# Kernel optimization log

Measured on AMD Instinct MI355X. Metric: run time of the kernel, lower is better.

## Reference

```python
import jax, jax.numpy as jnp
import numpy as np

VW, VD, VH = 96, 96, 96  # voxel_width, voxel_depth, voxel_height


def _grid_points():
    # voxel centers mapped to [-1, 1]: (2*i + 1 - N) / N
    xp = (2.0 * jnp.arange(VW) + 1.0 - VW) / VW
    yp = (2.0 * jnp.arange(VD) + 1.0 - VD) / VD
    zp = (2.0 * jnp.arange(VH) + 1.0 - VH) / VH
    X, Y, Z = jnp.meshgrid(xp, yp, zp, indexing='ij')
    return jnp.stack([X.ravel(), Y.ravel(), Z.ravel()], axis=-1)  # (V, 3)


def setup_inputs() -> dict:
    key = jax.random.key(0)
    k1, k2 = jax.random.split(key)
    B, NV, NF = 8, 2048, 512
    vertices = jax.random.uniform(k1, (B, NV, 3), dtype=jnp.float32, minval=-1.0, maxval=1.0)
    facets = jax.random.randint(k2, (B, NF, 4), 0, NV, dtype=jnp.int64)
    return {"vertices": vertices, "facets": facets}


def reference(vertices, facets):
    # vertices: (B, NV, 3) float32; facets: (B, NF, 4) int indices into vertices
    B = vertices.shape[0]
    NF = facets.shape[1]
    # vertices_to_facets: per-batch gather -> (B, NF, 4, 3)
    fverts = jax.vmap(lambda v, f: v[f])(vertices, facets)
    P = _grid_points()                      # (V, 3) voxel centers
    V = P.shape[0]

    def step(idx_map, xs):
        fi, verts = xs                      # verts: (B, 4, 3)
        v3 = verts[:, 3]                    # (B, 3)
        # T[:, j] = verts[j] - verts[3]  (columns are tetra edges)
        T = jnp.swapaxes(verts[:, :3] - v3[:, None, :], 1, 2)  # (B, 3, 3)
        a, b, c = T[:, 0, 0], T[:, 0, 1], T[:, 0, 2]
        d, e, f = T[:, 1, 0], T[:, 1, 1], T[:, 1, 2]
        g, h, i = T[:, 2, 0], T[:, 2, 1], T[:, 2, 2]
        # adjugate of T (matches t_inv_* in the original)
        adj = jnp.stack([
            jnp.stack([e * i - f * h, c * h - b * i, b * f - c * e], axis=-1),
            jnp.stack([f * g - d * i, a * i - c * g, c * d - a * f], axis=-1),
            jnp.stack([d * h - e * g, b * g - a * h, a * e - b * d], axis=-1),
        ], axis=1)                          # (B, 3, 3)
        det = a * (e * i - f * h) - b * (d * i - f * g) + c * (d * h - e * g)  # (B,)
        dvec = P[None, :, :] - v3[:, None, :]                  # (B, V, 3)
        lam = jnp.einsum('brc,bvc->bvr', adj, dvec) / det[:, None, None]  # (B, V, 3)
        lam4 = 1.0 - lam.sum(axis=-1, keepdims=True)
        lams = jnp.concatenate([lam, lam4], axis=-1)           # (B, V, 4)
        # original skips when any lambda < 0 or > 1 (strict) -> inside is inclusive
        inside = jnp.all((lams >= 0.0) & (lams <= 1.0), axis=-1)  # (B, V)
        idx_map = jnp.where((idx_map < 0) & inside, fi, idx_map)
        return idx_map, None

    idx0 = jnp.full((B, V), -1, dtype=jnp.int32)
    xs = (jnp.arange(NF, dtype=jnp.int32), jnp.swapaxes(fverts, 0, 1))
    idx_map, _ = jax.lax.scan(step, idx0, xs)
    alpha = (idx_map >= 0).astype(jnp.float32).reshape(B, VW, VD, VH)
    return alpha
```

## Files before the change

kernel.cpp:

```cpp
#include <hip/hip_runtime.h>

#pragma clang fp contract(off)

#define VWD 96
#define NVERT 2048
#define NFAC 512
#define NBATCH 8
#define NSLAB 3456
#define RECF 16
#define CULC 22

#define CUL(c, b, f) cul[(size_t)(c) * (NBATCH * NFAC) + (size_t)(b) * NFAC + (f)]

__global__ __launch_bounds__(512) void precompute_kernel(
    const float* __restrict__ vertices,
    const int*   __restrict__ facets,
    float*       __restrict__ cul,
    float*       __restrict__ body)
{
    __shared__ unsigned skey[NFAC];
    const int b = blockIdx.x;
    const int j = threadIdx.x;
    const float* vb = vertices + (size_t)b * NVERT * 3;

    int4 fi = ((const int4*)facets)[b * NFAC + j];
    float x0 = vb[3*fi.x+0], y0 = vb[3*fi.x+1], z0 = vb[3*fi.x+2];
    float x1 = vb[3*fi.y+0], y1 = vb[3*fi.y+1], z1 = vb[3*fi.y+2];
    float x2 = vb[3*fi.z+0], y2 = vb[3*fi.z+1], z2 = vb[3*fi.z+2];
    float x3 = vb[3*fi.w+0], y3 = vb[3*fi.w+1], z3 = vb[3*fi.w+2];
    float a  = x0-x3, bb = x1-x3, c  = x2-x3;
    float d  = y0-y3, e  = y1-y3, f  = y2-y3;
    float g  = z0-z3, h  = z1-z3, ii = z2-z3;
    float A00 = e*ii - f*h,  A01 = c*h  - bb*ii, A02 = bb*f - c*e;
    float A10 = f*g  - d*ii, A11 = a*ii - c*g,   A12 = c*d  - a*f;
    float A20 = d*h  - e*g,  A21 = bb*g - a*h,   A22 = a*e  - bb*d;
    float det = a*(e*ii - f*h) - bb*(d*ii - f*g) + c*(d*h - e*g);
    if (det < 0.0f) {
        det = -det;
        A00 = -A00; A01 = -A01; A02 = -A02;
        A10 = -A10; A11 = -A11; A12 = -A12;
        A20 = -A20; A21 = -A21; A22 = -A22;
    }
    unsigned myk = ~__float_as_uint(det);
    skey[j] = myk;
    __syncthreads();

    int rank = 0;
    const uint4* sk4 = (const uint4*)skey;
    for (int k0 = 0; k0 < NFAC; k0 += 4) {
        uint4 kk = sk4[k0 >> 2];
        rank += (kk.x < myk) + ((kk.x == myk) & (k0 + 0 < j));
        rank += (kk.y < myk) + ((kk.y == myk) & (k0 + 1 < j));
        rank += (kk.z < myk) + ((kk.z == myk) & (k0 + 2 < j));
        rank += (kk.w < myk) + ((kk.w == myk) & (k0 + 3 < j));
    }

    CUL(0, b, rank) = fminf(fminf(x0,x1),fminf(x2,x3)) - 1e-4f;
    CUL(1, b, rank) = fminf(fminf(y0,y1),fminf(y2,y3)) - 1e-4f;
    CUL(2, b, rank) = fminf(fminf(z0,z1),fminf(z2,z3)) - 1e-4f;
    CUL(3, b, rank) = fmaxf(fmaxf(x0,x1),fmaxf(x2,x3)) + 1e-4f;
    CUL(4, b, rank) = fmaxf(fmaxf(y0,y1),fmaxf(y2,y3)) + 1e-4f;
    CUL(5, b, rank) = fmaxf(fmaxf(z0,z1),fmaxf(z2,z3)) + 1e-4f;

    const float HX = 7.0f/96.0f, HZ = 3.0f/96.0f;
    auto plane = [&](float pax, float pay, float paz,
                     float pbx, float pby, float pbz,
                     float pcx, float pcy, float pcz,
                     float pox, float poy, float poz, int base) {
        float e1x = pbx-pax, e1y = pby-pay, e1z = pbz-paz;
        float e2x = pcx-pax, e2y = pcy-pay, e2z = pcz-paz;
        float nx = e1y*e2z - e1z*e2y;
        float ny = e1z*e2x - e1x*e2z;
        float nz = e1x*e2y - e1y*e2x;
        float sdot = nx*(pox-pax) + ny*(poy-pay) + nz*(poz-paz);
        if (sdot > 0.0f) { nx=-nx; ny=-ny; nz=-nz; sdot=-sdot; }
        float dpl = nx*pax + ny*pay + nz*paz;
        float n1s = fabsf(nx)+fabsf(ny)+fabsf(nz);
        float M = 1e-4f*(-sdot) + 1e-4f*n1s + 1e-4f;
        float rhs = dpl + M + (fabsf(nx)*HX + fabsf(ny)*HX + fabsf(nz)*HZ);
        CUL(base+0, b, rank) = nx;
        CUL(base+1, b, rank) = ny;
        CUL(base+2, b, rank) = nz;
        CUL(base+3, b, rank) = rhs;
    };
    plane(x1,y1,z1, x2,y2,z2, x3,y3,z3, x0,y0,z0, 6);
    plane(x0,y0,z0, x2,y2,z2, x3,y3,z3, x1,y1,z1, 10);
    plane(x0,y0,z0, x1,y1,z1, x3,y3,z3, x2,y2,z2, 14);
    plane(x0,y0,z0, x1,y1,z1, x2,y2,z2, x3,y3,z3, 18);

    float* bo = body + ((size_t)b * NFAC + rank) * RECF;
    bo[0]  = det; bo[1]  = x3;  bo[2]  = y3;  bo[3]  = z3;
    bo[4]  = A00; bo[5]  = A01; bo[6]  = A02; bo[7]  = A10;
    bo[8]  = A11; bo[9]  = A12; bo[10] = A20; bo[11] = A21;
    bo[12] = A22;
    bo[13] = det * (1.0f - 1e-5f) - 1e-25f;
    bo[14] = det * (1.0f + 1e-5f) + 1e-25f;
    bo[15] = 0.0f;
}

__global__ __launch_bounds__(512) void mask_kernel(
    const float* __restrict__ cul,
    unsigned long long* __restrict__ masks)
{
    const int col = blockIdx.x;
    const int b   = blockIdx.y;
    const int f   = threadIdx.x;
    const int w   = threadIdx.x >> 6;
    float bminx=CUL(0,b,f), bminy=CUL(1,b,f), bminz=CUL(2,b,f);
    float bmaxx=CUL(3,b,f), bmaxy=CUL(4,b,f), bmaxz=CUL(5,b,f);
    float n0x=CUL(6,b,f),  n0y=CUL(7,b,f),  n0z=CUL(8,b,f),  r0=CUL(9,b,f);
    float n1x=CUL(10,b,f), n1y=CUL(11,b,f), n1z=CUL(12,b,f), r1=CUL(13,b,f);
    float n2x=CUL(14,b,f), n2y=CUL(15,b,f), n2z=CUL(16,b,f), r2=CUL(17,b,f);
    float n3x=CUL(18,b,f), n3y=CUL(19,b,f), n3z=CUL(20,b,f), r3=CUL(21,b,f);

    const int sx = col / 12, sy = col % 12;
    const float cx = (float)(16*sx + 8 - VWD) / 96.0f;
    const float cy = (float)(16*sy + 8 - VWD) / 96.0f;
    const float colminx = (float)(16*sx + 1  - VWD) / 96.0f;
    const float colmaxx = (float)(16*sx + 15 - VWD) / 96.0f;
    const float colminy = (float)(16*sy + 1  - VWD) / 96.0f;
    const float colmaxy = (float)(16*sy + 15 - VWD) / 96.0f;
    const bool ovxy = (bminx <= colmaxx) & (bmaxx >= colminx) &
                      (bminy <= colmaxy) & (bmaxy >= colminy);

    const float cz0   = (float)(4 - VWD) / 96.0f;
    const float stepc = 8.0f / 96.0f;
    float d0 = n0x*cx + n0y*cy + n0z*cz0 - r0;  float s0 = n0z*stepc;
    float d1 = n1x*cx + n1y*cy + n1z*cz0 - r1;  float s1 = n1z*stepc;
    float d2 = n2x*cx + n2y*cy + n2z*cz0 - r2;  float s2 = n2z*stepc;
    float d3 = n3x*cx + n3y*cy + n3z*cz0 - r3;  float s3 = n3z*stepc;
    float zlo = (float)(1 - VWD) / 96.0f;
    float zhi = (float)(7 - VWD) / 96.0f;

    unsigned long long* mp = masks + ((size_t)b * NSLAB + (size_t)col * 24) * 8 + w;
#pragma unroll 4
    for (int sz = 0; sz < 24; ++sz) {
        bool ov = ovxy & (bminz <= zhi) & (bmaxz >= zlo) &
                  (d0 <= 0.0f) & (d1 <= 0.0f) & (d2 <= 0.0f) & (d3 <= 0.0f);
        unsigned long long bal = __ballot((int)ov);
        if ((threadIdx.x & 63) == 0) mp[(size_t)sz * 8] = bal;
        d0 += s0; d1 += s1; d2 += s2; d3 += s3;
        zlo += stepc; zhi += stepc;
    }
}

__global__ __launch_bounds__(128) void voxelize_kernel(
    const float*              __restrict__ body,
    const unsigned long long* __restrict__ masks,
    float*                    __restrict__ out)
{
    const int b    = blockIdx.y;
    const int wave = threadIdx.x >> 6;
    const int lane = threadIdx.x & 63;
    const int slab = blockIdx.x * 2 + wave;
    const int sz = slab % 24;
    const int sy = (slab / 24) % 12;
    const int sx = slab / 288;
    const int ix  = sx*8 + (lane >> 3);
    const int iy  = sy*8 + (lane & 7);
    const int iz0 = sz*4;

    const float px  = (float)(2*ix + 1 - VWD) / 96.0f;
    const float py  = (float)(2*iy + 1 - VWD) / 96.0f;
    const float pz0 = (float)(2*(iz0+0) + 1 - VWD) / 96.0f;
    const float pz1 = (float)(2*(iz0+1) + 1 - VWD) / 96.0f;
    const float pz2 = (float)(2*(iz0+2) + 1 - VWD) / 96.0f;
    const float pz3 = (float)(2*(iz0+3) + 1 - VWD) / 96.0f;

    const unsigned long long* mp = masks + ((size_t)b * NSLAB + slab) * 8;
    const float* bb = body + (size_t)b * NFAC * RECF;

    unsigned fnd = 0u;
    for (int w = 0; w < 8; ++w) {
        unsigned long long m = mp[w];
        while (m) {
            int bit = __builtin_ctzll(m);
            m &= m - 1;
            int f = __builtin_amdgcn_readfirstlane(w * 64 + bit);
            const float* bo = bb + f * RECF;
            float det = bo[0], v3x = bo[1], v3y = bo[2], v3z = bo[3];
            float A00 = bo[4],  A01 = bo[5],  A02 = bo[6],  A10 = bo[7];
            float A11 = bo[8],  A12 = bo[9],  A20 = bo[10], A21 = bo[11];
            float A22 = bo[12], dhi = bo[13], mhi = bo[14];
            float dx = px - v3x, dy = py - v3y;
            float p0 = A00*dx + A01*dy;
            float p1 = A10*dx + A11*dy;
            float p2 = A20*dx + A21*dy;
            float dzk0 = pz0 - v3z, dzk1 = pz1 - v3z;
            float dzk2 = pz2 - v3z, dzk3 = pz3 - v3z;
            unsigned need = 0u;
#pragma unroll
            for (int k = 0; k < 4; ++k) {
                float dzk = (k == 0) ? dzk0 : (k == 1) ? dzk1
                          : (k == 2) ? dzk2 : dzk3;
                float n0 = p0 + A02*dzk;
                float n1 = p1 + A12*dzk;
                float n2 = p2 + A22*dzk;
                float sm = (n0 + n1) + n2;
                float mn = fminf(fminf(n0, n1), n2);
                bool ge0 = (mn >= 0.0f);
                bool def = ge0 & (sm <= dhi);
                bool may = ge0 & (sm <= mhi);
                if (may & !def & !((fnd >> k) & 1u)) need |= (1u << k);
                if (def) fnd |= (1u << k);
            }
            if (__any(need != 0u)) {
#pragma unroll
                for (int k = 0; k < 4; ++k) {
                    float dzk = (k == 0) ? dzk0 : (k == 1) ? dzk1
                              : (k == 2) ? dzk2 : dzk3;
                    float n0 = p0 + A02*dzk;
                    float n1 = p1 + A12*dzk;
                    float n2 = p2 + A22*dzk;
                    float l0 = n0 / det;
                    float l1 = n1 / det;
                    float l2 = n2 / det;
                    float l3 = 1.0f - ((l0 + l1) + l2);
                    bool inside = (l0 >= 0.0f) & (l0 <= 1.0f) &
                                  (l1 >= 0.0f) & (l1 <= 1.0f) &
                                  (l2 >= 0.0f) & (l2 <= 1.0f) &
                                  (l3 >= 0.0f) & (l3 <= 1.0f);
                    if (((need >> k) & 1u) & inside) fnd |= (1u << k);
                }
            }
            if (__all(fnd == 15u)) goto done;
        }
    }
done:
    float4 v;
    v.x = (fnd & 1u) ? 1.0f : 0.0f;
    v.y = (fnd & 2u) ? 1.0f : 0.0f;
    v.z = (fnd & 4u) ? 1.0f : 0.0f;
    v.w = (fnd & 8u) ? 1.0f : 0.0f;
    *(float4*)&out[(size_t)b*(VWD*VWD*VWD) + (size_t)ix*(VWD*VWD) + iy*VWD + iz0] = v;
}

extern "C" void kernel_launch(void* const* d_in, const int* in_sizes, int n_in,
                              void* d_out, int out_size, void* d_ws, size_t ws_size,
                              hipStream_t stream) {
    const float* vertices = (const float*)d_in[0];
    const int*   facets   = (const int*)d_in[1];
    float*       out      = (float*)d_out;

    float* cul  = (float*)d_ws;
    float* body = (float*)((char*)d_ws + (size_t)CULC * NBATCH * NFAC * 4);
    unsigned long long* msk =
        (unsigned long long*)((char*)d_ws +
                              (size_t)(CULC + RECF) * NBATCH * NFAC * 4);

    precompute_kernel<<<NBATCH, 512, 0, stream>>>(vertices, facets, cul, body);
    mask_kernel<<<dim3(144, NBATCH), 512, 0, stream>>>(cul, msk);
    dim3 grid(NSLAB / 2, NBATCH);
    voxelize_kernel<<<grid, 128, 0, stream>>>(body, msk, out);
}
```

Baseline: 144.8 us.

## Skip fully covered slabs and defer high-index facets to a compacted fix-up kernel

The mask kernel now records, per column and z-slab, whether some tetrahedron's planes provably contain the whole slab, using per-plane margin thresholds computed in precompute. Such slabs are written as all-ones without any per-facet tests. The main voxelize kernel only walks the first 128 facet bits. Slabs that still have unresolved voxels and remaining candidates are appended to a global list via atomics, and a new fix-up kernel processes them with six waves splitting the remaining facet words and sharing results through LDS atomics. This aims to cut long serial facet walks and improve load balance, at the cost of an extra launch, atomics, and a conservative coverage test that must stay exact.

```diff
diff --git a/kernel.cpp b/kernel.cpp
--- a/kernel.cpp
+++ b/kernel.cpp
@@ -8,7 +8,7 @@
 #define NBATCH 8
 #define NSLAB 3456
 #define RECF 16
-#define CULC 22
+#define CULC 26
 
 #define CUL(c, b, f) cul[(size_t)(c) * (NBATCH * NFAC) + (size_t)(b) * NFAC + (f)]
 
@@ -16,11 +16,13 @@
     const float* __restrict__ vertices,
     const int*   __restrict__ facets,
     float*       __restrict__ cul,
-    float*       __restrict__ body)
+    float*       __restrict__ body,
+    unsigned*    __restrict__ scnt)
 {
     __shared__ unsigned skey[NFAC];
     const int b = blockIdx.x;
     const int j = threadIdx.x;
+    if (b == 0 && j == 0) scnt[0] = 0u;
     const float* vb = vertices + (size_t)b * NVERT * 3;
 
     int4 fi = ((const int4*)facets)[b * NFAC + j];
@@ -66,7 +68,7 @@
     auto plane = [&](float pax, float pay, float paz,
                      float pbx, float pby, float pbz,
                      float pcx, float pcy, float pcz,
-                     float pox, float poy, float poz, int base) {
+                     float pox, float poy, float poz, int base, int pi) {
         float e1x = pbx-pax, e1y = pby-pay, e1z = pbz-paz;
         float e2x = pcx-pax, e2y = pcy-pay, e2z = pcz-paz;
         float nx = e1y*e2z - e1z*e2y;
@@ -77,16 +79,18 @@
         float dpl = nx*pax + ny*pay + nz*paz;
         float n1s = fabsf(nx)+fabsf(ny)+fabsf(nz);
         float M = 1e-4f*(-sdot) + 1e-4f*n1s + 1e-4f;
-        float rhs = dpl + M + (fabsf(nx)*HX + fabsf(ny)*HX + fabsf(nz)*HZ);
+        float E = fabsf(nx)*HX + fabsf(ny)*HX + fabsf(nz)*HZ;
+        float rhs = dpl + M + E;
         CUL(base+0, b, rank) = nx;
         CUL(base+1, b, rank) = ny;
         CUL(base+2, b, rank) = nz;
         CUL(base+3, b, rank) = rhs;
+        CUL(22+pi, b, rank) = -(M + 2.0f*E + 2e-3f);
     };
-    plane(x1,y1,z1, x2,y2,z2, x3,y3,z3, x0,y0,z0, 6);
-    plane(x0,y0,z0, x2,y2,z2, x3,y3,z3, x1,y1,z1, 10);
-    plane(x0,y0,z0, x1,y1,z1, x3,y3,z3, x2,y2,z2, 14);
-    plane(x0,y0,z0, x1,y1,z1, x2,y2,z2, x3,y3,z3, 18);
+    plane(x1,y1,z1, x2,y2,z2, x3,y3,z3, x0,y0,z0, 6, 0);
+    plane(x0,y0,z0, x2,y2,z2, x3,y3,z3, x1,y1,z1, 10, 1);
+    plane(x0,y0,z0, x1,y1,z1, x3,y3,z3, x2,y2,z2, 14, 2);
+    plane(x0,y0,z0, x1,y1,z1, x2,y2,z2, x3,y3,z3, 18, 3);
 
     float* bo = body + ((size_t)b * NFAC + rank) * RECF;
     bo[0]  = det; bo[1]  = x3;  bo[2]  = y3;  bo[3]  = z3;
@@ -100,18 +104,23 @@
 
 __global__ __launch_bounds__(512) void mask_kernel(
     const float* __restrict__ cul,
-    unsigned long long* __restrict__ masks)
-{
+    unsigned long long* __restrict__ masks,
+    unsigned* __restrict__ fullmask)
+{
+    __shared__ unsigned fullbits;
     const int col = blockIdx.x;
     const int b   = blockIdx.y;
     const int f   = threadIdx.x;
     const int w   = threadIdx.x >> 6;
+    if (threadIdx.x == 0) fullbits = 0u;
+    __syncthreads();
     float bminx=CUL(0,b,f), bminy=CUL(1,b,f), bminz=CUL(2,b,f);
     float bmaxx=CUL(3,b,f), bmaxy=CUL(4,b,f), bmaxz=CUL(5,b,f);
     float n0x=CUL(6,b,f),  n0y=CUL(7,b,f),  n0z=CUL(8,b,f),  r0=CUL(9,b,f);
     float n1x=CUL(10,b,f), n1y=CUL(11,b,f), n1z=CUL(12,b,f), r1=CUL(13,b,f);
     float n2x=CUL(14,b,f), n2y=CUL(15,b,f), n2z=CUL(16,b,f), r2=CUL(17,b,f);
     float n3x=CUL(18,b,f), n3y=CUL(19,b,f), n3z=CUL(20,b,f), r3=CUL(21,b,f);
+    float D0=CUL(22,b,f), D1=CUL(23,b,f), D2=CUL(24,b,f), D3=CUL(25,b,f);
 
     const int sx = col / 12, sy = col % 12;
     const float cx = (float)(16*sx + 8 - VWD) / 96.0f;
@@ -132,29 +141,91 @@
     float zlo = (float)(1 - VWD) / 96.0f;
     float zhi = (float)(7 - VWD) / 96.0f;
 
+    unsigned fullw = 0u;
     unsigned long long* mp = masks + ((size_t)b * NSLAB + (size_t)col * 24) * 8 + w;
 #pragma unroll 4
     for (int sz = 0; sz < 24; ++sz) {
         bool ov = ovxy & (bminz <= zhi) & (bmaxz >= zlo) &
                   (d0 <= 0.0f) & (d1 <= 0.0f) & (d2 <= 0.0f) & (d3 <= 0.0f);
+        bool fullv = (d0 <= D0) & (d1 <= D1) & (d2 <= D2) & (d3 <= D3);
         unsigned long long bal = __ballot((int)ov);
         if ((threadIdx.x & 63) == 0) mp[(size_t)sz * 8] = bal;
+        if (__ballot((int)fullv) != 0ull) fullw |= (1u << sz);
         d0 += s0; d1 += s1; d2 += s2; d3 += s3;
         zlo += stepc; zhi += stepc;
+    }
+    if ((threadIdx.x & 63) == 0 && fullw) atomicOr(&fullbits, fullw);
+    __syncthreads();
+    if (threadIdx.x == 0) fullmask[b * 144 + col] = fullbits;
+}
+
+__device__ __forceinline__ void facet_test(
+    const float* __restrict__ bo,
+    float px, float py, float pz0, float pz1, float pz2, float pz3,
+    unsigned& fnd)
+{
+    float det = bo[0], v3x = bo[1], v3y = bo[2], v3z = bo[3];
+    float A00 = bo[4],  A01 = bo[5],  A02 = bo[6],  A10 = bo[7];
+    float A11 = bo[8],  A12 = bo[9],  A20 = bo[10], A21 = bo[11];
+    float A22 = bo[12], dhi = bo[13], mhi = bo[14];
+    float dx = px - v3x, dy = py - v3y;
+    float p0 = A00*dx + A01*dy;
+    float p1 = A10*dx + A11*dy;
+    float p2 = A20*dx + A21*dy;
+    float dzk0 = pz0 - v3z, dzk1 = pz1 - v3z;
+    float dzk2 = pz2 - v3z, dzk3 = pz3 - v3z;
+    unsigned need = 0u;
+#pragma unroll
+    for (int k = 0; k < 4; ++k) {
+        float dzk = (k == 0) ? dzk0 : (k == 1) ? dzk1
+                  : (k == 2) ? dzk2 : dzk3;
+        float n0 = p0 + A02*dzk;
+        float n1 = p1 + A12*dzk;
+        float n2 = p2 + A22*dzk;
+        float sm = (n0 + n1) + n2;
+        float mn = fminf(fminf(n0, n1), n2);
+        bool ge0 = (mn >= 0.0f);
+        bool def = ge0 & (sm <= dhi);
+        bool may = ge0 & (sm <= mhi);
+        if (may & !def & !((fnd >> k) & 1u)) need |= (1u << k);
+        if (def) fnd |= (1u << k);
+    }
+    if (__any(need != 0u)) {
+#pragma unroll
+        for (int k = 0; k < 4; ++k) {
+            float dzk = (k == 0) ? dzk0 : (k == 1) ? dzk1
+                      : (k == 2) ? dzk2 : dzk3;
+            float n0 = p0 + A02*dzk;
+            float n1 = p1 + A12*dzk;
+            float n2 = p2 + A22*dzk;
+            float l0 = n0 / det;
+            float l1 = n1 / det;
+            float l2 = n2 / det;
+            float l3 = 1.0f - ((l0 + l1) + l2);
+            bool inside = (l0 >= 0.0f) & (l0 <= 1.0f) &
+                          (l1 >= 0.0f) & (l1 <= 1.0f) &
+                          (l2 >= 0.0f) & (l2 <= 1.0f) &
+                          (l3 >= 0.0f) & (l3 <= 1.0f);
+            if (((need >> k) & 1u) & inside) fnd |= (1u << k);
+        }
     }
 }
 
 __global__ __launch_bounds__(128) void voxelize_kernel(
     const float*              __restrict__ body,
     const unsigned long long* __restrict__ masks,
-    float*                    __restrict__ out)
+    const unsigned*           __restrict__ fullmask,
+    float*                    __restrict__ out,
+    unsigned*                 __restrict__ scnt,
+    unsigned short*           __restrict__ slist)
 {
     const int b    = blockIdx.y;
     const int wave = threadIdx.x >> 6;
     const int lane = threadIdx.x & 63;
     const int slab = blockIdx.x * 2 + wave;
     const int sz = slab % 24;
-    const int sy = (slab / 24) % 12;
+    const int col = slab / 24;
+    const int sy = col % 12;
     const int sx = slab / 288;
     const int ix  = sx*8 + (lane >> 3);
     const int iy  = sy*8 + (lane & 7);
@@ -167,63 +238,30 @@
     const float pz2 = (float)(2*(iz0+2) + 1 - VWD) / 96.0f;
     const float pz3 = (float)(2*(iz0+3) + 1 - VWD) / 96.0f;
 
-    const unsigned long long* mp = masks + ((size_t)b * NSLAB + slab) * 8;
-    const float* bb = body + (size_t)b * NFAC * RECF;
-
     unsigned fnd = 0u;
-    for (int w = 0; w < 8; ++w) {
-        unsigned long long m = mp[w];
-        while (m) {
-            int bit = __builtin_ctzll(m);
-            m &= m - 1;
-            int f = __builtin_amdgcn_readfirstlane(w * 64 + bit);
-            const float* bo = bb + f * RECF;
-            float det = bo[0], v3x = bo[1], v3y = bo[2], v3z = bo[3];
-            float A00 = bo[4],  A01 = bo[5],  A02 = bo[6],  A10 = bo[7];
-            float A11 = bo[8],  A12 = bo[9],  A20 = bo[10], A21 = bo[11];
-            float A22 = bo[12], dhi = bo[13], mhi = bo[14];
-            float dx = px - v3x, dy = py - v3y;
-            float p0 = A00*dx + A01*dy;
-            float p1 = A10*dx + A11*dy;
-            float p2 = A20*dx + A21*dy;
-            float dzk0 = pz0 - v3z, dzk1 = pz1 - v3z;
-            float dzk2 = pz2 - v3z, dzk3 = pz3 - v3z;
-            unsigned need = 0u;
+
+    if ((fullmask[b * 144 + col] >> sz) & 1u) { fnd = 15u; goto done; }
+
+    {
+        const unsigned long long* mp = masks + ((size_t)b * NSLAB + slab) * 8;
+        const float* bb = body + (size_t)b * NFAC * RECF;
 #pragma unroll
-            for (int k = 0; k < 4; ++k) {
-                float dzk = (k == 0) ? dzk0 : (k == 1) ? dzk1
-                          : (k == 2) ? dzk2 : dzk3;
-                float n0 = p0 + A02*dzk;
-                float n1 = p1 + A12*dzk;
-                float n2 = p2 + A22*dzk;
-                float sm = (n0 + n1) + n2;
-                float mn = fminf(fminf(n0, n1), n2);
-                bool ge0 = (mn >= 0.0f);
-                bool def = ge0 & (sm <= dhi);
-                bool may = ge0 & (sm <= mhi);
-                if (may & !def & !((fnd >> k) & 1u)) need |= (1u << k);
-                if (def) fnd |= (1u << k);
+        for (int w = 0; w < 2; ++w) {
+            unsigned long long m = mp[w];
+            while (m) {
+                int bit = __builtin_ctzll(m);
+                m &= m - 1;
+                int f = __builtin_amdgcn_readfirstlane(w * 64 + bit);
+                facet_test(bb + f * RECF, px, py, pz0, pz1, pz2, pz3, fnd);
+                if (__all(fnd == 15u)) goto done;
             }
-            if (__any(need != 0u)) {
-#pragma unroll
-                for (int k = 0; k < 4; ++k) {
-                    float dzk = (k == 0) ? dzk0 : (k == 1) ? dzk1
-                              : (k == 2) ? dzk2 : dzk3;
-                    float n0 = p0 + A02*dzk;
-                    float n1 = p1 + A12*dzk;
-                    float n2 = p2 + A22*dzk;
-                    float l0 = n0 / det;
-                    float l1 = n1 / det;
-                    float l2 = n2 / det;
-                    float l3 = 1.0f - ((l0 + l1) + l2);
-                    bool inside = (l0 >= 0.0f) & (l0 <= 1.0f) &
-                                  (l1 >= 0.0f) & (l1 <= 1.0f) &
-                                  (l2 >= 0.0f) & (l2 <= 1.0f) &
-                                  (l3 >= 0.0f) & (l3 <= 1.0f);
-                    if (((need >> k) & 1u) & inside) fnd |= (1u << k);
-                }
+        }
+        unsigned long long rem = mp[2] | mp[3] | mp[4] | mp[5] | mp[6] | mp[7];
+        if (rem != 0ull && !__all(fnd == 15u)) {
+            if (lane == 0) {
+                unsigned idx = atomicAdd(scnt, 1u);
+                slist[idx] = (unsigned short)(b * NSLAB + slab);
             }
-            if (__all(fnd == 15u)) goto done;
         }
     }
 done:
@@ -235,6 +273,72 @@
     *(float4*)&out[(size_t)b*(VWD*VWD*VWD) + (size_t)ix*(VWD*VWD) + iy*VWD + iz0] = v;
 }
 
+__global__ __launch_bounds__(384) void voxelize_fix_kernel(
+    const float*              __restrict__ body,
+    const unsigned long long* __restrict__ masks,
+    float*                    __restrict__ out,
+    const unsigned*           __restrict__ scnt,
+    const unsigned short*     __restrict__ slist)
+{
+    __shared__ unsigned fl[64];
+    const int wave = threadIdx.x >> 6;
+    const int lane = threadIdx.x & 63;
+    const unsigned count = *scnt;
+
+    for (unsigned e = blockIdx.x; e < count; e += gridDim.x) {
+        const int v    = (int)slist[e];
+        const int b    = v / NSLAB;
+        const int slab = v % NSLAB;
+        const int sz = slab % 24;
+        const int sy = (slab / 24) % 12;
+        const int sx = slab / 288;
+        const int ix  = sx*8 + (lane >> 3);
+        const int iy  = sy*8 + (lane & 7);
+        const int iz0 = sz*4;
+        const float px  = (float)(2*ix + 1 - VWD) / 96.0f;
+        const float py  = (float)(2*iy + 1 - VWD) / 96.0f;
+        const float pz0 = (float)(2*(iz0+0) + 1 - VWD) / 96.0f;
+        const float pz1 = (float)(2*(iz0+1) + 1 - VWD) / 96.0f;
+        const float pz2 = (float)(2*(iz0+2) + 1 - VWD) / 96.0f;
+        const float pz3 = (float)(2*(iz0+3) + 1 - VWD) / 96.0f;
+        float* op = &out[(size_t)b*(VWD*VWD*VWD) + (size_t)ix*(VWD*VWD) + iy*VWD + iz0];
+
+        __syncthreads();
+        if (threadIdx.x < 64) {
+            float4 o = *(const float4*)op;
+            fl[threadIdx.x] = (o.x != 0.0f ? 1u : 0u) | (o.y != 0.0f ? 2u : 0u)
+                            | (o.z != 0.0f ? 4u : 0u) | (o.w != 0.0f ? 8u : 0u);
+        }
+        __syncthreads();
+
+        unsigned fnd = fl[lane];
+        unsigned pub = fnd;
+        const unsigned long long* mp = masks + ((size_t)b * NSLAB + slab) * 8;
+        const float* bb = body + (size_t)b * NFAC * RECF;
+        unsigned long long m = mp[2 + wave];
+        while (m) {
+            int bit = __builtin_ctzll(m);
+            m &= m - 1;
+            int f = __builtin_amdgcn_readfirstlane((2 + wave) * 64 + bit);
+            facet_test(bb + f * RECF, px, py, pz0, pz1, pz2, pz3, fnd);
+            if (fnd != pub) { atomicOr(&fl[lane], fnd); pub = fnd; }
+            fnd |= fl[lane];
+            if (__all(fnd == 15u)) break;
+        }
+        if (fnd != pub) atomicOr(&fl[lane], fnd);
+        __syncthreads();
+        if (threadIdx.x < 64) {
+            unsigned u = fl[threadIdx.x];
+            float4 r;
+            r.x = (u & 1u) ? 1.0f : 0.0f;
+            r.y = (u & 2u) ? 1.0f : 0.0f;
+            r.z = (u & 4u) ? 1.0f : 0.0f;
+            r.w = (u & 8u) ? 1.0f : 0.0f;
+            *(float4*)op = r;
+        }
+    }
+}
+
 extern "C" void kernel_launch(void* const* d_in, const int* in_sizes, int n_in,
                               void* d_out, int out_size, void* d_ws, size_t ws_size,
                               hipStream_t stream) {
@@ -243,13 +347,15 @@
     float*       out      = (float*)d_out;
 
     float* cul  = (float*)d_ws;
-    float* body = (float*)((char*)d_ws + (size_t)CULC * NBATCH * NFAC * 4);
-    unsigned long long* msk =
-        (unsigned long long*)((char*)d_ws +
-                              (size_t)(CULC + RECF) * NBATCH * NFAC * 4);
-
-    precompute_kernel<<<NBATCH, 512, 0, stream>>>(vertices, facets, cul, body);
-    mask_kernel<<<dim3(144, NBATCH), 512, 0, stream>>>(cul, msk);
+    float* body = (float*)((char*)d_ws + 425984);
+    unsigned long long* msk = (unsigned long long*)((char*)d_ws + 688128);
+    unsigned* fullmask = (unsigned*)((char*)d_ws + 2457600);
+    unsigned* scnt     = (unsigned*)((char*)d_ws + 2462208);
+    unsigned short* slist = (unsigned short*)((char*)d_ws + 2462272);
+
+    precompute_kernel<<<NBATCH, 512, 0, stream>>>(vertices, facets, cul, body, scnt);
+    mask_kernel<<<dim3(144, NBATCH), 512, 0, stream>>>(cul, msk, fullmask);
     dim3 grid(NSLAB / 2, NBATCH);
-    voxelize_kernel<<<grid, 128, 0, stream>>>(body, msk, out);
-}
+    voxelize_kernel<<<grid, 128, 0, stream>>>(body, msk, fullmask, out, scnt, slist);
+    voxelize_fix_kernel<<<1024, 384, 0, stream>>>(body, msk, out, scnt, slist);
+}
```

Measured after the change: 359.1 us. 2.48x slower.
